# Kernel optimization log

Hardware: AMD Instinct MI355X
Metric: run time of the kernel (lower is better)

Reference implementation:

```python
import jax, jax.numpy as jnp
import numpy as np

N_NODES = 100_000
N_EDGES = 1_600_000
IN_DIM = 500
HID = 128
OUT = 16
DEG = 3          # Chebyshev 'order' -> DEG+1 basis terms
N_KAN_USED = 2   # forward applies kan_layers[:num_layers-1] with num_layers=3


def spmm(edge_index, h):
    # torch.sparse.mm(A, h) with A = COO(edge_index, ones, (N, N)):
    # out[row] = sum over edges of h[col]
    return jax.ops.segment_sum(h[edge_index[1]], edge_index[0], num_segments=N_NODES)


def cheb_kan(h, coeffs):
    # ChebyKANLayer: t = tanh(h); basis T_k(t) = cos(k*arccos(t)) computed via
    # the (mathematically identical, numerically stable) recurrence.
    t = jnp.tanh(h)                                  # [N, HID]
    Ts = [jnp.ones_like(t), t]
    for _ in range(DEG - 1):
        Ts.append(2.0 * t * Ts[-1] - Ts[-2])
    basis = jnp.stack(Ts, axis=-1)                   # [N, HID, DEG+1]
    return jnp.einsum('nid,iod->no', basis, coeffs)  # [N, HID]


def setup_inputs() -> dict:
    key = jax.random.key(0)
    ks = jax.random.split(key, 6)
    x = jax.random.normal(ks[0], (N_NODES, IN_DIM), dtype=jnp.float32)
    edge_index = jax.random.randint(ks[1], (2, N_EDGES), 0, N_NODES)
    W_in = jax.random.normal(ks[2], (IN_DIM, HID), dtype=jnp.float32) / np.sqrt(IN_DIM)
    cheb_coeffs = jax.random.normal(ks[3], (N_KAN_USED, HID, HID, DEG + 1),
                                    dtype=jnp.float32) / (HID * (DEG + 1))
    W_out = jax.random.normal(ks[4], (HID, OUT), dtype=jnp.float32) / np.sqrt(HID)
    return {"x": x, "edge_index": edge_index, "W_in": W_in,
            "cheb_coeffs": cheb_coeffs, "W_out": W_out}


def reference(x, edge_index, W_in, cheb_coeffs, W_out):
    h = x @ W_in                      # linear_input (no bias)
    # dropout is identity at inference
    h = spmm(edge_index, h)           # sparse adjacency aggregation
    for l in range(N_KAN_USED):
        h = cheb_kan(h, cheb_coeffs[l])
        h = spmm(edge_index, h)
    logits = h @ W_out                # output_layer (no bias)
    return jax.nn.log_softmax(logits, axis=-1)
```

## Files before the change

### kernel.cpp

```cpp
#include <hip/hip_runtime.h>
#include <hip/hip_bf16.h>

#define N_NODES 100000
#define N_EDGES 1600000
#define IN_DIM  500
#define HID     128
#define KDIM    512
#define NB      782
#define BCAP    4096

typedef __attribute__((ext_vector_type(8))) short bf16x8;
typedef __attribute__((ext_vector_type(4))) float f32x4;

__device__ inline short f2bf(float x) {
    union { float f; unsigned u; } v; v.f = x;
    unsigned r = (v.u + 0x7FFFu + ((v.u >> 16) & 1u)) >> 16;
    return (short)r;
}
__device__ inline float bf_lo(unsigned u) { union { unsigned u; float f; } v; v.u = u << 16; return v.f; }
__device__ inline float bf_hi(unsigned u) { union { unsigned u; float f; } v; v.u = u & 0xFFFF0000u; return v.f; }

__device__ inline bf16x8 cheb_frag(unsigned v) {
    float hx[2] = {bf_lo(v), bf_hi(v)};
    short t[8];
#pragma unroll
    for (int q = 0; q < 2; q++) {
        float xx = fminf(fmaxf(hx[q], -15.f), 15.f);
        float e  = __expf(2.f * xx);
        float tt = (e - 1.f) / (e + 1.f);
        float T2 = 2.f * tt * tt - 1.f;
        float T3 = 2.f * tt * T2 - tt;
        t[q * 4 + 0] = (short)0x3F80;
        t[q * 4 + 1] = f2bf(tt);
        t[q * 4 + 2] = f2bf(T2);
        t[q * 4 + 3] = f2bf(T3);
    }
    return *(bf16x8*)&t[0];
}


__global__ __launch_bounds__(256) void bin_kernel(const int* __restrict__ ei,
                                                  int* __restrict__ bcnt,
                                                  unsigned* __restrict__ buf) {
    int e = blockIdx.x * 256 + threadIdx.x;
    if (e < N_EDGES) {
        int r = ei[e];
        int c = ei[N_EDGES + e];
        int b = r >> 7;
        int p = atomicAdd(&bcnt[b * 16], 1);
        if (p < BCAP) buf[b * BCAP + p] = ((unsigned)(r & 127) << 17) | (unsigned)c;
    }
}

__global__ __launch_bounds__(1024) void bscan_kernel(const int* __restrict__ bcnt,
                                                     int* __restrict__ bbase) {
    __shared__ int buf[1024];
    const int tid = threadIdx.x;
    int v = (tid < NB) ? bcnt[tid * 16] : 0;
    buf[tid] = v;
    __syncthreads();
    for (int off = 1; off < 1024; off <<= 1) {
        int t = (tid >= off) ? buf[tid - off] : 0;
        __syncthreads();
        buf[tid] += t;
        __syncthreads();
    }
    if (tid < NB) bbase[tid] = buf[tid] - v;
}

__global__ __launch_bounds__(256) void place_kernel(const unsigned* __restrict__ buf,
                                                    const int* __restrict__ bcnt,
                                                    const int* __restrict__ bbase,
                                                    int* __restrict__ row_start,
                                                    int* __restrict__ col_sorted) {
    __shared__ int hist[128];
    __shared__ int scan[128];
    __shared__ int cur[128];
    const int b = blockIdx.x, tid = threadIdx.x;
    int cnt = bcnt[b * 16]; if (cnt > BCAP) cnt = BCAP;
    const int base = bbase[b];
    if (tid < 128) hist[tid] = 0;
    __syncthreads();
    for (int i = tid; i < cnt; i += 256)
        atomicAdd(&hist[buf[b * BCAP + i] >> 17], 1);
    __syncthreads();
    if (tid < 128) scan[tid] = hist[tid];
    __syncthreads();
    for (int off = 1; off < 128; off <<= 1) {
        int t = (tid < 128 && tid >= off) ? scan[tid - off] : 0;
        __syncthreads();
        if (tid < 128) scan[tid] += t;
        __syncthreads();
    }
    if (tid < 128) {
        int excl = scan[tid] - hist[tid] + base;
        cur[tid] = excl;
        int r = b * 128 + tid;
        if (r < N_NODES) row_start[r] = excl;
        if (r == N_NODES - 1) row_start[N_NODES] = excl + hist[tid];
    }
    __syncthreads();
    for (int i = tid; i < cnt; i += 256) {
        unsigned u = buf[b * BCAP + i];
        int rl = (int)(u >> 17);
        int c  = (int)(u & 0x1FFFFu);
        int pos = atomicAdd(&cur[rl], 1);
        col_sorted[pos] = c;
    }
}

__global__ __launch_bounds__(256) void repack_all(const float* __restrict__ cheb,
                                                  const float* __restrict__ W,
                                                  const float* __restrict__ Wout,
                                                  unsigned short* __restrict__ Bmat,
                                                  unsigned short* __restrict__ Wmat,
                                                  unsigned short* __restrict__ C2W) {
    const int b = blockIdx.x;
    if (b < 256) {
        int idx = b * 256 + threadIdx.x;
        int o = idx >> 9;
        int k = idx & 511;
        int i = k >> 2;
        int d = k & 3;
        Bmat[idx] = (unsigned short)f2bf(cheb[i * 512 + o * 4 + d]);
    } else if (b < 512) {
        int idx = (b - 256) * 256 + threadIdx.x;
        int o = idx >> 9;
        int k = idx & 511;
        Wmat[idx] = (k < IN_DIM) ? (unsigned short)f2bf(W[k * HID + o]) : 0;
    } else {
        int idx = (b - 512) * 256 + threadIdx.x;
        int o16 = idx >> 9;
        int k   = idx & 511;
        const float* cb = cheb + 65536 + (k >> 2) * 512 + (k & 3);
        float s = 0.f;
#pragma unroll 4
        for (int o = 0; o < 128; o++) s += cb[o * 4] * Wout[o * 16 + o16];
        C2W[o16 * 512 + k] = (unsigned short)f2bf(s);
    }
}

__global__ __launch_bounds__(256, 4) void gemm_xw(const float* __restrict__ x,
                                                  const unsigned short* __restrict__ Wmat,
                                                  unsigned short* __restrict__ out) {
    __shared__ __align__(16) short Bs[2][128][40];
    const int tid  = threadIdx.x;
    const int lane = tid & 63;
    const int wave = tid >> 6;
    const int quad = lane >> 4;
    const int l16  = lane & 15;
    const int n0   = blockIdx.x * 64;
    const int br   = tid >> 1;
    const int bh   = tid & 1;

    int row = n0 + wave * 16 + l16; if (row >= N_NODES) row = N_NODES - 1;
    const float* __restrict__ xrow = x + (long)row * IN_DIM;

    f32x4 acc[8];
#pragma unroll
    for (int nt = 0; nt < 8; nt++)
#pragma unroll
        for (int r = 0; r < 4; r++) acc[nt][r] = 0.f;

    auto loadA = [&](int kt, float (&v)[8]) {
        const int kb = kt * 32 + quad * 8;
        if (kb + 8 <= IN_DIM) {
            const float4* s4 = (const float4*)(xrow + kb);
            float4 a0 = s4[0], a1 = s4[1];
            v[0]=a0.x; v[1]=a0.y; v[2]=a0.z; v[3]=a0.w;
            v[4]=a1.x; v[5]=a1.y; v[6]=a1.z; v[7]=a1.w;
        } else {
#pragma unroll
            for (int q = 0; q < 8; q++) v[q] = (kb + q < IN_DIM) ? xrow[kb + q] : 0.f;
        }
    };
    auto loadB = [&](int kt, bf16x8 (&w)[2]) {
        w[0] = *(const bf16x8*)&Wmat[br * 512 + kt * 32 + bh * 16];
        w[1] = *(const bf16x8*)&Wmat[br * 512 + kt * 32 + bh * 16 + 8];
    };
    auto storeB = [&](int buf, const bf16x8 (&w)[2]) {
        *(bf16x8*)&Bs[buf][br][bh * 16]     = w[0];
        *(bf16x8*)&Bs[buf][br][bh * 16 + 8] = w[1];
    };
    auto mfmaTile = [&](int buf, const float (&v)[8]) {
        short t[8];
#pragma unroll
        for (int q = 0; q < 8; q++) t[q] = f2bf(v[q]);
        bf16x8 a = *(bf16x8*)&t[0];
#pragma unroll
        for (int nt = 0; nt < 8; nt++) {
            bf16x8 b = *(const bf16x8*)&Bs[buf][nt * 16 + l16][quad * 8];
            acc[nt] = __builtin_amdgcn_mfma_f32_16x16x32_bf16(a, b, acc[nt], 0, 0, 0);
        }
    };

    float  va[8], vb[8];
    bf16x8 wa[2], wb[2];
    loadA(0, va); loadB(0, wa);
    for (int kt = 0; kt < 16; kt += 2) {
        storeB(0, wa);
        loadB(kt + 1, wb);
        loadA(kt + 1, vb);
        __syncthreads();
        mfmaTile(0, va);
        storeB(1, wb);
        if (kt + 2 < 16) { loadB(kt + 2, wa); loadA(kt + 2, va); }
        __syncthreads();
        mfmaTile(1, vb);
    }

    {
        int mrow = n0 + wave * 16 + quad * 4;
#pragma unroll
        for (int r = 0; r < 4; r++) {
            int n = mrow + r;
            if (n < N_NODES) {
#pragma unroll
                for (int nt = 0; nt < 8; nt++)
                    out[(long)n * HID + nt * 16 + l16] = (unsigned short)f2bf(acc[nt][r]);
            }
        }
    }
}

__global__ __launch_bounds__(256, 4) void cheb_gemm(const unsigned short* __restrict__ h,
                                                    const unsigned short* __restrict__ Bmat,
                                                    unsigned short* __restrict__ out) {
    __shared__ __align__(16) short Bs[2][128][40];
    const int tid  = threadIdx.x;
    const int lane = tid & 63;
    const int wave = tid >> 6;
    const int quad = lane >> 4;
    const int l16  = lane & 15;
    const int n0   = blockIdx.x * 64;
    const int br   = tid >> 1;
    const int bh   = tid & 1;

    int row = n0 + wave * 16 + l16; if (row >= N_NODES) row = N_NODES - 1;
    const unsigned short* __restrict__ hrow = h + (long)row * HID;

    unsigned hreg[16];
#pragma unroll
    for (int kt = 0; kt < 16; kt++)
        hreg[kt] = *(const unsigned*)(hrow + kt * 8 + quad * 2);

    f32x4 acc[8];
#pragma unroll
    for (int nt = 0; nt < 8; nt++)
#pragma unroll
        for (int r = 0; r < 4; r++) acc[nt][r] = 0.f;

    auto loadB = [&](int kt, bf16x8 (&w)[2]) {
        w[0] = *(const bf16x8*)&Bmat[br * 512 + kt * 32 + bh * 16];
        w[1] = *(const bf16x8*)&Bmat[br * 512 + kt * 32 + bh * 16 + 8];
    };
    auto storeB = [&](int buf, const bf16x8 (&w)[2]) {
        *(bf16x8*)&Bs[buf][br][bh * 16]     = w[0];
        *(bf16x8*)&Bs[buf][br][bh * 16 + 8] = w[1];
    };
    auto mfmaTile = [&](int buf, int kt) {
        bf16x8 a = cheb_frag(hreg[kt]);
#pragma unroll
        for (int nt = 0; nt < 8; nt++) {
            bf16x8 b = *(const bf16x8*)&Bs[buf][nt * 16 + l16][quad * 8];
            acc[nt] = __builtin_amdgcn_mfma_f32_16x16x32_bf16(a, b, acc[nt], 0, 0, 0);
        }
    };

    bf16x8 wa[2], wb[2];
    loadB(0, wa);
    for (int kt = 0; kt < 16; kt += 2) {
        storeB(0, wa);
        loadB(kt + 1, wb);
        __syncthreads();
        mfmaTile(0, kt);
        storeB(1, wb);
        if (kt + 2 < 16) loadB(kt + 2, wa);
        __syncthreads();
        mfmaTile(1, kt + 1);
    }

    {
        int mrow = n0 + wave * 16 + quad * 4;
#pragma unroll
        for (int r = 0; r < 4; r++) {
            int n = mrow + r;
            if (n < N_NODES) {
#pragma unroll
                for (int nt = 0; nt < 8; nt++)
                    out[(long)n * HID + nt * 16 + l16] = (unsigned short)f2bf(acc[nt][r]);
            }
        }
    }
}

__global__ __launch_bounds__(256, 4) void cheb16_gemm(const unsigned short* __restrict__ h,
                                                      const unsigned short* __restrict__ C2W,
                                                      float* __restrict__ z) {
    __shared__ __align__(16) short Bs16[16][520];
    const int tid  = threadIdx.x;
    const int lane = tid & 63;
    const int wave = tid >> 6;
    const int quad = lane >> 4;
    const int l16  = lane & 15;
    const int n0   = blockIdx.x * 64;

    {
        int o16 = tid >> 4;
        int seg = tid & 15;
        *(bf16x8*)&Bs16[o16][seg * 32]      = *(const bf16x8*)&C2W[o16 * 512 + seg * 32];
        *(bf16x8*)&Bs16[o16][seg * 32 + 8]  = *(const bf16x8*)&C2W[o16 * 512 + seg * 32 + 8];
        *(bf16x8*)&Bs16[o16][seg * 32 + 16] = *(const bf16x8*)&C2W[o16 * 512 + seg * 32 + 16];
        *(bf16x8*)&Bs16[o16][seg * 32 + 24] = *(const bf16x8*)&C2W[o16 * 512 + seg * 32 + 24];
    }

    int row = n0 + wave * 16 + l16; if (row >= N_NODES) row = N_NODES - 1;
    const unsigned short* __restrict__ hrow = h + (long)row * HID;

    unsigned hreg[16];
#pragma unroll
    for (int kt = 0; kt < 16; kt++)
        hreg[kt] = *(const unsigned*)(hrow + kt * 8 + quad * 2);

    f32x4 acc;
#pragma unroll
    for (int r = 0; r < 4; r++) acc[r] = 0.f;

    __syncthreads();

#pragma unroll
    for (int kt = 0; kt < 16; kt++) {
        bf16x8 a = cheb_frag(hreg[kt]);
        bf16x8 b = *(const bf16x8*)&Bs16[l16][kt * 32 + quad * 8];
        acc = __builtin_amdgcn_mfma_f32_16x16x32_bf16(a, b, acc, 0, 0, 0);
    }

    {
        int mrow = n0 + wave * 16 + quad * 4;
#pragma unroll
        for (int r = 0; r < 4; r++) {
            int n = mrow + r;
            if (n < N_NODES) z[n * 16 + l16] = acc[r];
        }
    }
}

__global__ __launch_bounds__(256) void spmm_gather(const int* __restrict__ row_start,
                                                   const int* __restrict__ col_sorted,
                                                   const unsigned short* __restrict__ h,
                                                   unsigned short* __restrict__ out) {
    const int wid  = (blockIdx.x * 256 + threadIdx.x) >> 6;
    const int lane = threadIdx.x & 63;
    const int sub  = lane >> 4;
    const int fl   = lane & 15;
    if (wid >= N_NODES) return;
    const int s = row_start[wid];
    const int e = row_start[wid + 1];
    const uint4* __restrict__ h4 = (const uint4*)h;

    float a[8], b[8];
#pragma unroll
    for (int q = 0; q < 8; q++) { a[q] = 0.f; b[q] = 0.f; }

    int j = s;
    for (; j + 8 <= e; j += 8) {
        int c0 = col_sorted[j + sub];
        int c1 = col_sorted[j + 4 + sub];
        uint4 u0 = h4[c0 * 16 + fl];
        uint4 u1 = h4[c1 * 16 + fl];
        a[0] += bf_lo(u0.x); a[1] += bf_hi(u0.x);
        a[2] += bf_lo(u0.y); a[3] += bf_hi(u0.y);
        a[4] += bf_lo(u0.z); a[5] += bf_hi(u0.z);
        a[6] += bf_lo(u0.w); a[7] += bf_hi(u0.w);
        b[0] += bf_lo(u1.x); b[1] += bf_hi(u1.x);
        b[2] += bf_lo(u1.y); b[3] += bf_hi(u1.y);
        b[4] += bf_lo(u1.z); b[5] += bf_hi(u1.z);
        b[6] += bf_lo(u1.w); b[7] += bf_hi(u1.w);
    }
    for (; j < e; j += 4) {
        int idx = j + sub;
        float m = (idx < e) ? 1.f : 0.f;
        int ci = (idx < e) ? idx : (e - 1);
        int c = col_sorted[ci];
        uint4 u = h4[c * 16 + fl];
        a[0] = fmaf(m, bf_lo(u.x), a[0]); a[1] = fmaf(m, bf_hi(u.x), a[1]);
        a[2] = fmaf(m, bf_lo(u.y), a[2]); a[3] = fmaf(m, bf_hi(u.y), a[3]);
        a[4] = fmaf(m, bf_lo(u.z), a[4]); a[5] = fmaf(m, bf_hi(u.z), a[5]);
        a[6] = fmaf(m, bf_lo(u.w), a[6]); a[7] = fmaf(m, bf_hi(u.w), a[7]);
    }
#pragma unroll
    for (int q = 0; q < 8; q++) a[q] += b[q];
#pragma unroll
    for (int q = 0; q < 8; q++) {
        a[q] += __shfl_xor(a[q], 16);
        a[q] += __shfl_xor(a[q], 32);
    }
    if (sub == 0) {
        unsigned w0 = (unsigned)(unsigned short)f2bf(a[0]) | ((unsigned)(unsigned short)f2bf(a[1]) << 16);
        unsigned w1 = (unsigned)(unsigned short)f2bf(a[2]) | ((unsigned)(unsigned short)f2bf(a[3]) << 16);
        unsigned w2 = (unsigned)(unsigned short)f2bf(a[4]) | ((unsigned)(unsigned short)f2bf(a[5]) << 16);
        unsigned w3 = (unsigned)(unsigned short)f2bf(a[6]) | ((unsigned)(unsigned short)f2bf(a[7]) << 16);
        uint4 pw; pw.x = w0; pw.y = w1; pw.z = w2; pw.w = w3;
        ((uint4*)out)[wid * 16 + fl] = pw;
    }
}

__global__ __launch_bounds__(256) void spmm_out(const int* __restrict__ row_start,
                                                const int* __restrict__ col_sorted,
                                                const float* __restrict__ z,
                                                float* __restrict__ out) {
    const int wid  = (blockIdx.x * 256 + threadIdx.x) >> 6;
    const int lane = threadIdx.x & 63;
    const int sub  = lane >> 4;
    const int fl   = lane & 15;
    if (wid >= N_NODES) return;
    const int s = row_start[wid];
    const int e = row_start[wid + 1];

    float a0 = 0.f, a1 = 0.f;
    int j = s;
    for (; j + 8 <= e; j += 8) {
        int c0 = col_sorted[j + sub];
        int c1 = col_sorted[j + 4 + sub];
        a0 += z[c0 * 16 + fl];
        a1 += z[c1 * 16 + fl];
    }
    for (; j < e; j += 4) {
        int idx = j + sub;
        float m = (idx < e) ? 1.f : 0.f;
        int ci = (idx < e) ? idx : (e - 1);
        a0 = fmaf(m, z[col_sorted[ci] * 16 + fl], a0);
    }
    float v = a0 + a1;
    v += __shfl_xor(v, 16);
    v += __shfl_xor(v, 32);
    float mx = v;
#pragma unroll
    for (int m = 8; m >= 1; m >>= 1) mx = fmaxf(mx, __shfl_xor(mx, m));
    float ex = expf(v - mx);
    float se = ex;
#pragma unroll
    for (int m = 8; m >= 1; m >>= 1) se += __shfl_xor(se, m);
    if (sub == 0) out[wid * 16 + fl] = v - mx - logf(se);
}


extern "C" void kernel_launch(void* const* d_in, const int* in_sizes, int n_in,
                              void* d_out, int out_size, void* d_ws, size_t ws_size,
                              hipStream_t stream) {
    const float* x     = (const float*)d_in[0];
    const int*   ei    = (const int*)d_in[1];
    const float* W_in  = (const float*)d_in[2];
    const float* cheb  = (const float*)d_in[3];
    const float* W_out = (const float*)d_in[4];
    float* out = (float*)d_out;

    char* p = (char*)d_ws;
    unsigned short* hA   = (unsigned short*)p; p += (size_t)N_NODES * HID * 2;
    unsigned short* hB   = (unsigned short*)p; p += (size_t)N_NODES * HID * 2;
    int*   col_sorted    = (int*)p;            p += (size_t)N_EDGES * 4;
    unsigned short* Bmat = (unsigned short*)p; p += (size_t)HID * KDIM * 2;
    unsigned short* Wmat = (unsigned short*)p; p += (size_t)HID * KDIM * 2;
    unsigned short* C2W  = (unsigned short*)p; p += (size_t)16 * KDIM * 2;
    float* zbuf          = (float*)p;          p += (size_t)N_NODES * 16 * 4;
    int*   row_start     = (int*)p;            p += (size_t)(N_NODES + 1) * 4;
    int*   bcnt          = (int*)p;            p += (size_t)NB * 16 * 4;
    int*   bbase         = (int*)p;            p += (size_t)NB * 4;

    unsigned* bbuf = (unsigned*)hA;

    const int nblk_gemm = (N_NODES + 63) / 64;
    const int nblk_edge = N_EDGES / 256;
    const int nblk_spmm = (N_NODES + 3) / 4;

    hipMemsetAsync(bcnt, 0, (size_t)NB * 16 * 4, stream);
    bin_kernel<<<nblk_edge, 256, 0, stream>>>(ei, bcnt, bbuf);
    bscan_kernel<<<1, 1024, 0, stream>>>(bcnt, bbase);
    place_kernel<<<NB, 256, 0, stream>>>(bbuf, bcnt, bbase, row_start, col_sorted);
    repack_all<<<544, 256, 0, stream>>>(cheb, W_in, W_out, Bmat, Wmat, C2W);

    gemm_xw<<<nblk_gemm, 256, 0, stream>>>(x, Wmat, hA);
    spmm_gather<<<nblk_spmm, 256, 0, stream>>>(row_start, col_sorted, hA, hB);

    cheb_gemm<<<nblk_gemm, 256, 0, stream>>>(hB, Bmat, hA);
    spmm_gather<<<nblk_spmm, 256, 0, stream>>>(row_start, col_sorted, hA, hB);

    cheb16_gemm<<<nblk_gemm, 256, 0, stream>>>(hB, C2W, zbuf);
    spmm_out<<<nblk_spmm, 256, 0, stream>>>(row_start, col_sorted, zbuf, out);
}
```

Measured before the change: 645.4 us.

## Fuse edge binning into input GEMM launch and drop global bucket scan

```diff
diff --git a/kernel.cpp b/kernel.cpp
--- a/kernel.cpp
+++ b/kernel.cpp
@@ -8,6 +8,9 @@
 #define KDIM    512
 #define NB      782
 #define BCAP    4096
+
+#define NG_GEMM 1563
+#define NG_BIN  6250
 
 typedef __attribute__((ext_vector_type(8))) short bf16x8;
 typedef __attribute__((ext_vector_type(4))) float f32x4;
@@ -36,77 +39,6 @@
         t[q * 4 + 3] = f2bf(T3);
     }
     return *(bf16x8*)&t[0];
-}
-
-
-__global__ __launch_bounds__(256) void bin_kernel(const int* __restrict__ ei,
-                                                  int* __restrict__ bcnt,
-                                                  unsigned* __restrict__ buf) {
-    int e = blockIdx.x * 256 + threadIdx.x;
-    if (e < N_EDGES) {
-        int r = ei[e];
-        int c = ei[N_EDGES + e];
-        int b = r >> 7;
-        int p = atomicAdd(&bcnt[b * 16], 1);
-        if (p < BCAP) buf[b * BCAP + p] = ((unsigned)(r & 127) << 17) | (unsigned)c;
-    }
-}
-
-__global__ __launch_bounds__(1024) void bscan_kernel(const int* __restrict__ bcnt,
-                                                     int* __restrict__ bbase) {
-    __shared__ int buf[1024];
-    const int tid = threadIdx.x;
-    int v = (tid < NB) ? bcnt[tid * 16] : 0;
-    buf[tid] = v;
-    __syncthreads();
-    for (int off = 1; off < 1024; off <<= 1) {
-        int t = (tid >= off) ? buf[tid - off] : 0;
-        __syncthreads();
-        buf[tid] += t;
-        __syncthreads();
-    }
-    if (tid < NB) bbase[tid] = buf[tid] - v;
-}
-
-__global__ __launch_bounds__(256) void place_kernel(const unsigned* __restrict__ buf,
-                                                    const int* __restrict__ bcnt,
-                                                    const int* __restrict__ bbase,
-                                                    int* __restrict__ row_start,
-                                                    int* __restrict__ col_sorted) {
-    __shared__ int hist[128];
-    __shared__ int scan[128];
-    __shared__ int cur[128];
-    const int b = blockIdx.x, tid = threadIdx.x;
-    int cnt = bcnt[b * 16]; if (cnt > BCAP) cnt = BCAP;
-    const int base = bbase[b];
-    if (tid < 128) hist[tid] = 0;
-    __syncthreads();
-    for (int i = tid; i < cnt; i += 256)
-        atomicAdd(&hist[buf[b * BCAP + i] >> 17], 1);
-    __syncthreads();
-    if (tid < 128) scan[tid] = hist[tid];
-    __syncthreads();
-    for (int off = 1; off < 128; off <<= 1) {
-        int t = (tid < 128 && tid >= off) ? scan[tid - off] : 0;
-        __syncthreads();
-        if (tid < 128) scan[tid] += t;
-        __syncthreads();
-    }
-    if (tid < 128) {
-        int excl = scan[tid] - hist[tid] + base;
-        cur[tid] = excl;
-        int r = b * 128 + tid;
-        if (r < N_NODES) row_start[r] = excl;
-        if (r == N_NODES - 1) row_start[N_NODES] = excl + hist[tid];
-    }
-    __syncthreads();
-    for (int i = tid; i < cnt; i += 256) {
-        unsigned u = buf[b * BCAP + i];
-        int rl = (int)(u >> 17);
-        int c  = (int)(u & 0x1FFFFu);
-        int pos = atomicAdd(&cur[rl], 1);
-        col_sorted[pos] = c;
-    }
 }
 
 __global__ __launch_bounds__(256) void repack_all(const float* __restrict__ cheb,
@@ -140,76 +72,80 @@
     }
 }
 
-__global__ __launch_bounds__(256, 4) void gemm_xw(const float* __restrict__ x,
-                                                  const unsigned short* __restrict__ Wmat,
-                                                  unsigned short* __restrict__ out) {
+__global__ __launch_bounds__(256, 4) void prep_kernel(const float* __restrict__ x,
+                                                      const int* __restrict__ ei,
+                                                      const unsigned short* __restrict__ Wmat,
+                                                      unsigned short* __restrict__ hA,
+                                                      int* __restrict__ bcnt,
+                                                      unsigned* __restrict__ bbuf) {
     __shared__ __align__(16) short Bs[2][128][40];
-    const int tid  = threadIdx.x;
-    const int lane = tid & 63;
-    const int wave = tid >> 6;
-    const int quad = lane >> 4;
-    const int l16  = lane & 15;
-    const int n0   = blockIdx.x * 64;
-    const int br   = tid >> 1;
-    const int bh   = tid & 1;
-
-    int row = n0 + wave * 16 + l16; if (row >= N_NODES) row = N_NODES - 1;
-    const float* __restrict__ xrow = x + (long)row * IN_DIM;
-
-    f32x4 acc[8];
-#pragma unroll
-    for (int nt = 0; nt < 8; nt++)
-#pragma unroll
-        for (int r = 0; r < 4; r++) acc[nt][r] = 0.f;
-
-    auto loadA = [&](int kt, float (&v)[8]) {
-        const int kb = kt * 32 + quad * 8;
-        if (kb + 8 <= IN_DIM) {
-            const float4* s4 = (const float4*)(xrow + kb);
-            float4 a0 = s4[0], a1 = s4[1];
-            v[0]=a0.x; v[1]=a0.y; v[2]=a0.z; v[3]=a0.w;
-            v[4]=a1.x; v[5]=a1.y; v[6]=a1.z; v[7]=a1.w;
-        } else {
-#pragma unroll
-            for (int q = 0; q < 8; q++) v[q] = (kb + q < IN_DIM) ? xrow[kb + q] : 0.f;
-        }
-    };
-    auto loadB = [&](int kt, bf16x8 (&w)[2]) {
-        w[0] = *(const bf16x8*)&Wmat[br * 512 + kt * 32 + bh * 16];
-        w[1] = *(const bf16x8*)&Wmat[br * 512 + kt * 32 + bh * 16 + 8];
-    };
-    auto storeB = [&](int buf, const bf16x8 (&w)[2]) {
-        *(bf16x8*)&Bs[buf][br][bh * 16]     = w[0];
-        *(bf16x8*)&Bs[buf][br][bh * 16 + 8] = w[1];
-    };
-    auto mfmaTile = [&](int buf, const float (&v)[8]) {
-        short t[8];
-#pragma unroll
-        for (int q = 0; q < 8; q++) t[q] = f2bf(v[q]);
-        bf16x8 a = *(bf16x8*)&t[0];
-#pragma unroll
-        for (int nt = 0; nt < 8; nt++) {
-            bf16x8 b = *(const bf16x8*)&Bs[buf][nt * 16 + l16][quad * 8];
-            acc[nt] = __builtin_amdgcn_mfma_f32_16x16x32_bf16(a, b, acc[nt], 0, 0, 0);
-        }
-    };
-
-    float  va[8], vb[8];
-    bf16x8 wa[2], wb[2];
-    loadA(0, va); loadB(0, wa);
-    for (int kt = 0; kt < 16; kt += 2) {
-        storeB(0, wa);
-        loadB(kt + 1, wb);
-        loadA(kt + 1, vb);
-        __syncthreads();
-        mfmaTile(0, va);
-        storeB(1, wb);
-        if (kt + 2 < 16) { loadB(kt + 2, wa); loadA(kt + 2, va); }
-        __syncthreads();
-        mfmaTile(1, vb);
-    }
-
-    {
+    const int tid = threadIdx.x;
+
+    if (blockIdx.x < NG_GEMM) {
+        const int lane = tid & 63;
+        const int wave = tid >> 6;
+        const int quad = lane >> 4;
+        const int l16  = lane & 15;
+        const int n0   = blockIdx.x * 64;
+        const int br   = tid >> 1;
+        const int bh   = tid & 1;
+
+        int row = n0 + wave * 16 + l16; if (row >= N_NODES) row = N_NODES - 1;
+        const float* __restrict__ xrow = x + (long)row * IN_DIM;
+
+        f32x4 acc[8];
+#pragma unroll
+        for (int nt = 0; nt < 8; nt++)
+#pragma unroll
+            for (int r = 0; r < 4; r++) acc[nt][r] = 0.f;
+
+        auto loadA = [&](int kt, float (&v)[8]) {
+            const int kb = kt * 32 + quad * 8;
+            if (kb + 8 <= IN_DIM) {
+                const float4* s4 = (const float4*)(xrow + kb);
+                float4 a0 = s4[0], a1 = s4[1];
+                v[0]=a0.x; v[1]=a0.y; v[2]=a0.z; v[3]=a0.w;
+                v[4]=a1.x; v[5]=a1.y; v[6]=a1.z; v[7]=a1.w;
+            } else {
+#pragma unroll
+                for (int q = 0; q < 8; q++) v[q] = (kb + q < IN_DIM) ? xrow[kb + q] : 0.f;
+            }
+        };
+        auto loadB = [&](int kt, bf16x8 (&w)[2]) {
+            w[0] = *(const bf16x8*)&Wmat[br * 512 + kt * 32 + bh * 16];
+            w[1] = *(const bf16x8*)&Wmat[br * 512 + kt * 32 + bh * 16 + 8];
+        };
+        auto storeB = [&](int buf, const bf16x8 (&w)[2]) {
+            *(bf16x8*)&Bs[buf][br][bh * 16]     = w[0];
+            *(bf16x8*)&Bs[buf][br][bh * 16 + 8] = w[1];
+        };
+        auto mfmaTile = [&](int buf, const float (&v)[8]) {
+            short t[8];
+#pragma unroll
+            for (int q = 0; q < 8; q++) t[q] = f2bf(v[q]);
+            bf16x8 a = *(bf16x8*)&t[0];
+#pragma unroll
+            for (int nt = 0; nt < 8; nt++) {
+                bf16x8 b = *(const bf16x8*)&Bs[buf][nt * 16 + l16][quad * 8];
+                acc[nt] = __builtin_amdgcn_mfma_f32_16x16x32_bf16(a, b, acc[nt], 0, 0, 0);
+            }
+        };
+
+        float  va[8], vb[8];
+        bf16x8 wa[2], wb[2];
+        loadA(0, va); loadB(0, wa);
+        for (int kt = 0; kt < 16; kt += 2) {
+            storeB(0, wa);
+            loadB(kt + 1, wb);
+            loadA(kt + 1, vb);
+            __syncthreads();
+            mfmaTile(0, va);
+            storeB(1, wb);
+            if (kt + 2 < 16) { loadB(kt + 2, wa); loadA(kt + 2, va); }
+            __syncthreads();
+            mfmaTile(1, vb);
+        }
+
         int mrow = n0 + wave * 16 + quad * 4;
 #pragma unroll
         for (int r = 0; r < 4; r++) {
@@ -217,9 +153,62 @@
             if (n < N_NODES) {
 #pragma unroll
                 for (int nt = 0; nt < 8; nt++)
-                    out[(long)n * HID + nt * 16 + l16] = (unsigned short)f2bf(acc[nt][r]);
+                    hA[(long)n * HID + nt * 16 + l16] = (unsigned short)f2bf(acc[nt][r]);
             }
         }
+    } else {
+        int e = (blockIdx.x - NG_GEMM) * 256 + tid;
+        if (e < N_EDGES) {
+            int r = ei[e];
+            int c = ei[N_EDGES + e];
+            int b = r >> 7;
+            int p = atomicAdd(&bcnt[b * 16], 1);
+            if (p < BCAP) bbuf[b * BCAP + p] = ((unsigned)(r & 127) << 17) | (unsigned)c;
+        }
+    }
+}
+
+__global__ __launch_bounds__(256) void place_kernel(const unsigned* __restrict__ buf,
+                                                    const int* __restrict__ bcnt,
+                                                    int* __restrict__ gctr,
+                                                    int* __restrict__ row_start,
+                                                    int* __restrict__ row_cnt,
+                                                    int* __restrict__ col_sorted) {
+    __shared__ int hist[128];
+    __shared__ int scan[128];
+    __shared__ int cur[128];
+    __shared__ int base_s;
+    const int b = blockIdx.x, tid = threadIdx.x;
+    int cnt = bcnt[b * 16]; if (cnt > BCAP) cnt = BCAP;
+    if (tid < 128) hist[tid] = 0;
+    __syncthreads();
+    for (int i = tid; i < cnt; i += 256)
+        atomicAdd(&hist[buf[b * BCAP + i] >> 17], 1);
+    __syncthreads();
+    if (tid < 128) scan[tid] = hist[tid];
+    __syncthreads();
+    for (int off = 1; off < 128; off <<= 1) {
+        int t = (tid < 128 && tid >= off) ? scan[tid - off] : 0;
+        __syncthreads();
+        if (tid < 128) scan[tid] += t;
+        __syncthreads();
+    }
+    if (tid == 0) base_s = atomicAdd(gctr, scan[127]);
+    __syncthreads();
+    const int base = base_s;
+    if (tid < 128) {
+        int excl = scan[tid] - hist[tid] + base;
+        cur[tid] = excl;
+        int r = b * 128 + tid;
+        if (r < N_NODES) { row_start[r] = excl; row_cnt[r] = hist[tid]; }
+    }
+    __syncthreads();
+    for (int i = tid; i < cnt; i += 256) {
+        unsigned u = buf[b * BCAP + i];
+        int rl = (int)(u >> 17);
+        int c  = (int)(u & 0x1FFFFu);
+        int pos = atomicAdd(&cur[rl], 1);
+        col_sorted[pos] = c;
     }
 }
 
@@ -346,6 +335,7 @@
 }
 
 __global__ __launch_bounds__(256) void spmm_gather(const int* __restrict__ row_start,
+                                                   const int* __restrict__ row_cnt,
                                                    const int* __restrict__ col_sorted,
                                                    const unsigned short* __restrict__ h,
                                                    unsigned short* __restrict__ out) {
@@ -355,7 +345,7 @@
     const int fl   = lane & 15;
     if (wid >= N_NODES) return;
     const int s = row_start[wid];
-    const int e = row_start[wid + 1];
+    const int e = s + row_cnt[wid];
     const uint4* __restrict__ h4 = (const uint4*)h;
 
     float a[8], b[8];
@@ -406,6 +396,7 @@
 }
 
 __global__ __launch_bounds__(256) void spmm_out(const int* __restrict__ row_start,
+                                                const int* __restrict__ row_cnt,
                                                 const int* __restrict__ col_sorted,
                                                 const float* __restrict__ z,
                                                 float* __restrict__ out) {
@@ -415,7 +406,7 @@
     const int fl   = lane & 15;
     if (wid >= N_NODES) return;
     const int s = row_start[wid];
-    const int e = row_start[wid + 1];
+    const int e = s + row_cnt[wid];
 
     float a0 = 0.f, a1 = 0.f;
     int j = s;
@@ -463,28 +454,30 @@
     unsigned short* Wmat = (unsigned short*)p; p += (size_t)HID * KDIM * 2;
     unsigned short* C2W  = (unsigned short*)p; p += (size_t)16 * KDIM * 2;
     float* zbuf          = (float*)p;          p += (size_t)N_NODES * 16 * 4;
-    int*   row_start     = (int*)p;            p += (size_t)(N_NODES + 1) * 4;
-    int*   bcnt          = (int*)p;            p += (size_t)NB * 16 * 4;
-    int*   bbase         = (int*)p;            p += (size_t)NB * 4;
-
-    unsigned* bbuf = (unsigned*)hA;
-
+    int*   row_start     = (int*)p;            p += (size_t)N_NODES * 4;
+    int*   row_cnt       = (int*)p;            p += (size_t)N_NODES * 4;
+    int*   bcnt          = (int*)p;            p += (size_t)(NB * 16 + 16) * 4;
+
+    int* gctr = bcnt + NB * 16;
+
+    unsigned* bbuf = (unsigned*)hB;
+
+    const int nblk_prep = NG_GEMM + NG_BIN;
     const int nblk_gemm = (N_NODES + 63) / 64;
-    const int nblk_edge = N_EDGES / 256;
     const int nblk_spmm = (N_NODES + 3) / 4;
 
-    hipMemsetAsync(bcnt, 0, (size_t)NB * 16 * 4, stream);
-    bin_kernel<<<nblk_edge, 256, 0, stream>>>(ei, bcnt, bbuf);
-    bscan_kernel<<<1, 1024, 0, stream>>>(bcnt, bbase);
-    place_kernel<<<NB, 256, 0, stream>>>(bbuf, bcnt, bbase, row_start, col_sorted);
+    hipMemsetAsync(bcnt, 0, (size_t)(NB * 16 + 16) * 4, stream);
+
     repack_all<<<544, 256, 0, stream>>>(cheb, W_in, W_out, Bmat, Wmat, C2W);
 
-    gemm_xw<<<nblk_gemm, 256, 0, stream>>>(x, Wmat, hA);
-    spmm_gather<<<nblk_spmm, 256, 0, stream>>>(row_start, col_sorted, hA, hB);
+    prep_kernel<<<nblk_prep, 256, 0, stream>>>(x, ei, Wmat, hA, bcnt, bbuf);
+    place_kernel<<<NB, 256, 0, stream>>>(bbuf, bcnt, gctr, row_start, row_cnt, col_sorted);
+
+    spmm_gather<<<nblk_spmm, 256, 0, stream>>>(row_start, row_cnt, col_sorted, hA, hB);
 
     cheb_gemm<<<nblk_gemm, 256, 0, stream>>>(hB, Bmat, hA);
-    spmm_gather<<<nblk_spmm, 256, 0, stream>>>(row_start, col_sorted, hA, hB);
+    spmm_gather<<<nblk_spmm, 256, 0, stream>>>(row_start, row_cnt, col_sorted, hA, hB);
 
     cheb16_gemm<<<nblk_gemm, 256, 0, stream>>>(hB, C2W, zbuf);
-    spmm_out<<<nblk_spmm, 256, 0, stream>>>(row_start, col_sorted, zbuf, out);
-}
+    spmm_out<<<nblk_spmm, 256, 0, stream>>>(row_start, row_cnt, col_sorted, zbuf, out);
+}
```

Result: faster. 626.0 us (-3.0%).
